# Kernel tuning notes

Hardware: AMD Instinct MI355X
Metric: run time of the kernel (lower is better)

## Reference

```python
import jax, jax.numpy as jnp
import numpy as np
from jax import lax

B, C, L, O, H, W = 256, 768, 64, 768, 9, 9
C2, C3 = 2 * C // 3, C // 3  # convh_2 / convl_1 output channels


def _c1x1(x, w, b):
    # 1x1 conv, w: (out,in), x: (b,in,h,w)
    return jnp.einsum('oc,bchw->bohw', w, x) + b[None, :, None, None]


def _conv3x3(x, w, b=None):
    out = lax.conv_general_dilated(x, w, (1, 1), 'SAME', dimension_numbers=('NCHW', 'OIHW', 'NCHW'))
    if b is not None:
        out = out + b[None, :, None, None]
    return out


def _cossim(a, b):
    # torch F.cosine_similarity over dim=1, eps=1e-8
    num = jnp.sum(a * b, axis=1)
    den = jnp.maximum(jnp.linalg.norm(a, axis=1) * jnp.linalg.norm(b, axis=1), 1e-8)
    return num / den


def _ufilt1d(x, size, axis):
    # scipy.ndimage.uniform_filter1d, mode='reflect' (== numpy 'symmetric')
    r = size // 2
    pad = [(r, r) if a == axis else (0, 0) for a in range(x.ndim)]
    xp = jnp.moveaxis(jnp.pad(x, pad, mode='symmetric'), axis, -1)
    c = jnp.cumsum(xp, axis=-1)
    c = jnp.concatenate([jnp.zeros_like(c[..., :1]), c], axis=-1)
    out = (c[..., size:] - c[..., :-size]) / size
    return jnp.moveaxis(out, -1, axis)


def _ufilt(x, size):
    # skimage ssim with channel_axis=1 on a (b,c,h,w) array treats (b,h,w) as
    # the 3 spatial dims (batch included!) and loops over channels.
    for ax in (0, 2, 3):
        x = _ufilt1d(x, size, ax)
    return x


def _ssim_map(x, y, win=7):
    NP = win ** 3  # 3 spatial dims (b,h,w)
    cov_norm = NP / (NP - 1.0)
    c1, c2 = 0.01 ** 2, 0.03 ** 2  # data_range = 1.0
    ux, uy = _ufilt(x, win), _ufilt(y, win)
    vx = cov_norm * (_ufilt(x * x, win) - ux * ux)
    vy = cov_norm * (_ufilt(y * y, win) - uy * uy)
    vxy = cov_norm * (_ufilt(x * y, win) - ux * uy)
    return ((2 * ux * uy + c1) * (2 * vxy + c2)) / ((ux * ux + uy * uy + c1) * (vx + vy + c2))


def setup_inputs() -> dict:
    key = jax.random.key(0)
    ks = jax.random.split(key, 40)
    n = lambda i, shape, s=1.0: jax.random.normal(ks[i], shape, jnp.float32) * s
    return {
        'x': n(0, (B, C, H, W)),
        'y': n(1, (B, L, H, W)),
        'w_convh1': n(2, (C, C), C ** -0.5), 'b_convh1': n(3, (C,), 0.01),
        'w_conv1_1': n(4, (C, C), C ** -0.5), 'b_conv1_1': n(5, (C,), 0.01),
        'w_convh2': n(6, (C2, C), C ** -0.5), 'b_convh2': n(7, (C2,), 0.01),
        'w_convl1': n(8, (C3, L), L ** -0.5), 'b_convl1': n(9, (C3,), 0.01),
        'w_convh3': n(10, (1, C), C ** -0.5), 'b_convh3': n(11, (1,), 0.01),
        'w_convl2': n(12, (1, L), L ** -0.5), 'b_convl2': n(13, (1,), 0.01),
        'w_conv1_2': n(14, (2, 2), 0.7), 'b_conv1_2': n(15, (2,), 0.01),
        'w_convl3': n(16, (2, L), L ** -0.5), 'b_convl3': n(17, (2,), 0.01),
        'w_cc1': n(18, (1, 2), 0.7), 'b_cc1': n(19, (1,), 0.01),
        'w_pool': n(20, (2, 1, 3, 3), 1.0 / 3.0), 'b_pool': n(21, (2,), 0.01),
        'w_fc1': n(22, (324, 324), 324 ** -0.5), 'b_fc1': n(23, (324,), 0.01),
        'w_fc2': n(24, (81, 324), 324 ** -0.5), 'b_fc2': n(25, (81,), 0.01),
        'w_bconv': n(26, (O, C, 3, 3), (C * 9) ** -0.5),
        'bn_gamma': 1.0 + n(27, (O,), 0.1), 'bn_beta': n(28, (O,), 0.1),
        'bn_mean': n(29, (O,), 0.1),
        'bn_var': 1.0 + 0.1 * jax.random.uniform(ks[30], (O,), jnp.float32),
    }


def reference(x, y, w_convh1, b_convh1, w_conv1_1, b_conv1_1, w_convh2, b_convh2,
              w_convl1, b_convl1, w_convh3, b_convh3, w_convl2, b_convl2,
              w_conv1_2, b_conv1_2, w_convl3, b_convl3, w_cc1, b_cc1,
              w_pool, b_pool, w_fc1, b_fc1, w_fc2, b_fc2,
              w_bconv, bn_gamma, bn_beta, bn_mean, bn_var):
    b = x.shape[0]
    fuse_1 = _c1x1(x, w_convh1, b_convh1)                                   # (b,C,9,9)
    fuse_2 = _c1x1(jnp.concatenate([_c1x1(x, w_convh2, b_convh2),
                                    _c1x1(y, w_convl1, b_convl1)], axis=1),
                   w_conv1_1, b_conv1_1)                                     # (b,C,9,9)
    fuse_3 = _c1x1(jnp.concatenate([_c1x1(x, w_convh3, b_convh3),
                                    _c1x1(y, w_convl2, b_convl2)], axis=1),
                   w_conv1_2, b_conv1_2)                                     # (b,2,9,9)
    fuse_4 = _c1x1(y, w_convl3, b_convl3)                                    # (b,2,9,9)
    cor_1 = _cossim(fuse_1, fuse_2)[:, None]                                 # (b,1,9,9)
    ssim_value = lax.stop_gradient(_ssim_map(fuse_3, fuse_4))                # detach() in torch
    fuse2_1 = fuse_1 + 0.5 * (1.0 - cor_1) * fuse_2
    fuse2_2 = _c1x1(fuse_4 + ssim_value * fuse_3, w_cc1, b_cc1)              # (b,1,9,9)
    cor2_1 = _cossim(fuse2_1, jnp.broadcast_to(fuse2_2, fuse2_1.shape))[:, None]
    fuse3_1 = fuse2_1 + 0.5 * (1.0 - cor2_1 + _c1x1(ssim_value, w_cc1, b_cc1)) * fuse2_2
    # fuse2_2 has 1 channel -> channel mean == channel max == fuse2_2
    xc = jnp.concatenate([fuse2_2, _conv3x3(fuse2_2, w_pool, b_pool), fuse2_2], axis=1)  # (b,4,9,9)
    xc = xc.reshape(b, -1)
    h1 = jax.nn.gelu(xc @ w_fc1.T + b_fc1, approximate=False)
    xweight = jax.nn.leaky_relu(h1 @ w_fc2.T + b_fc2, 0.01).reshape(b, 1, H, W)
    xout = xweight * fuse3_1 + fuse3_1
    xout = _conv3x3(xout, w_bconv)
    scale = (bn_gamma / jnp.sqrt(bn_var + 1e-5))[None, :, None, None]
    xout = (xout - bn_mean[None, :, None, None]) * scale + bn_beta[None, :, None, None]
    return jax.nn.leaky_relu(xout, 0.01)
```

## Files before the change

### kernel.cpp

```cpp
#include <hip/hip_runtime.h>
#include <hip/hip_bf16.h>
#include <math.h>

#define BATCH 256
#define CCH 768
#define LCH 64
#define PP 81

typedef __attribute__((ext_vector_type(8))) short short8v;
typedef __attribute__((ext_vector_type(4))) float f32x4;

__global__ __launch_bounds__(256) void kw_compose(
    const float* __restrict__ W11, const float* __restrict__ Wh2,
    const float* __restrict__ Wl1, const float* __restrict__ bh2,
    const float* __restrict__ bl1, const float* __restrict__ b11,
    const float* __restrict__ Wh1,
    __hip_bfloat16* __restrict__ WAp, __hip_bfloat16* __restrict__ WBp,
    __hip_bfloat16* __restrict__ Wh1p, float* __restrict__ beff)
{
    int o = blockIdx.x;
    int t = threadIdx.x;
    int ot = o >> 4, l15o = o & 15;
    const float* w11row = W11 + (size_t)o * CCH;
    for (int c = t; c < CCH; c += 256) {
        float s = 0.f;
        for (int k = 0; k < 512; ++k) s = fmaf(w11row[k], Wh2[(size_t)k*CCH + c], s);
        int ch = c >> 5, kg = (c >> 3) & 3, j = c & 7;
        size_t idx = (((size_t)ot*24 + ch) << 9) + (size_t)(kg*16 + l15o)*8 + j;
        WAp[idx]  = __float2bfloat16(s);
        Wh1p[idx] = __float2bfloat16(Wh1[(size_t)o*CCH + c]);
    }
    if (t < LCH) {
        float s = 0.f;
        for (int k = 0; k < 256; ++k) s = fmaf(w11row[512+k], Wl1[k*LCH + t], s);
        int ch = t >> 5, kg = (t >> 3) & 3, j = t & 7;
        size_t idx = (((size_t)ot*2 + ch) << 9) + (size_t)(kg*16 + l15o)*8 + j;
        WBp[idx] = __float2bfloat16(s);
    }
    if (t == 0) {
        float s = b11[o];
        for (int k = 0; k < 512; ++k) s = fmaf(w11row[k], bh2[k], s);
        for (int k = 0; k < 256; ++k) s = fmaf(w11row[512+k], bl1[k], s);
        beff[o] = s;
    }
}

__global__ __launch_bounds__(256) void k_wprep(
    const float* __restrict__ Wb, __hip_bfloat16* __restrict__ Wp)
{
    int ot = blockIdx.x;
    int i  = blockIdx.y*256 + threadIdx.x;
    int oi = i / 96, c8 = i - oi*96;
    const float* src = Wb + ((size_t)(ot*16 + oi)*CCH + c8*8)*9;
    int ch = c8 >> 2;
    int lane8 = (((c8 & 3)*16) + oi)*8;
    #pragma unroll
    for (int t = 0; t < 9; ++t) {
        short8v v;
        #pragma unroll
        for (int j = 0; j < 8; ++j) {
            __hip_bfloat16 h = __float2bfloat16(src[j*9 + t]);
            v[j] = __builtin_bit_cast(short, h);
        }
        *(short8v*)(Wp + ((((size_t)(t*48 + ot))*24 + ch) << 9) + lane8) = v;
    }
}

__global__ __launch_bounds__(256) void k_fcprep(
    const float* __restrict__ Wfc1, const float* __restrict__ Wfc2,
    float* __restrict__ T1, float* __restrict__ T2)
{
    int n = blockIdx.x*256 + threadIdx.x;
    if (n < 324*324) { int i = n / 324, j = n - i*324; T1[(size_t)j*324 + i] = Wfc1[n]; }
    if (n < 81*324)  { int q = n / 324, j = n - q*324; T2[(size_t)j*81 + q]  = Wfc2[n]; }
}

__global__ __launch_bounds__(256) void k_xprep_f34(
    const float* __restrict__ x, const float* __restrict__ y,
    const float* __restrict__ wh3, const float* __restrict__ bh3,
    const float* __restrict__ wl2, const float* __restrict__ bl2,
    const float* __restrict__ W12, const float* __restrict__ b12,
    const float* __restrict__ Wl3, const float* __restrict__ bl3,
    __hip_bfloat16* __restrict__ xT, __hip_bfloat16* __restrict__ yT,
    float* __restrict__ f3, float* __restrict__ f4, float* __restrict__ Af)
{
    int b = blockIdx.x;
    int tid = threadIdx.x;
    __shared__ float ls[64][82];
    __shared__ float red[243][4];
    __shared__ float zz[10][81];
    __shared__ float tb[10][81];
    int q = tid / 81, p81 = tid - q*81;
    bool act = tid < 243;
    float sx = 0.f;
    for (int c0 = 0; c0 < CCH; c0 += 64) {
        __syncthreads();
        for (int i = tid; i < 64*81; i += 256) {
            int c = i / 81, p = i - c*81;
            ls[c][p] = x[((size_t)b*CCH + c0 + c)*PP + p];
        }
        __syncthreads();
        for (int i = tid; i < 81*64; i += 256) {
            int p = i >> 6, c = i & 63;
            xT[((size_t)b*PP + p)*CCH + c0 + c] = __float2bfloat16(ls[c][p]);
        }
        if (act)
            for (int c = q; c < 64; c += 3)
                sx = fmaf(wh3[c0+c], ls[c][p81], sx);
    }
    __syncthreads();
    for (int i = tid; i < 64*81; i += 256) {
        int c = i / 81, p = i - c*81;
        ls[c][p] = y[((size_t)b*LCH + c)*PP + p];
    }
    __syncthreads();
    for (int i = tid; i < 81*64; i += 256) {
        int p = i >> 6, c = i & 63;
        yT[((size_t)b*PP + p)*LCH + c] = __float2bfloat16(ls[c][p]);
    }
    float sy = 0.f, s40 = 0.f, s41 = 0.f;
    if (act) {
        for (int c = q; c < 64; c += 3) {
            float v = ls[c][p81];
            sy  = fmaf(wl2[c], v, sy);
            s40 = fmaf(Wl3[c], v, s40);
            s41 = fmaf(Wl3[LCH+c], v, s41);
        }
        red[tid][0]=sx; red[tid][1]=sy; red[tid][2]=s40; red[tid][3]=s41;
    }
    __syncthreads();
    if (tid < 81) {
        float SX  = red[tid][0]+red[tid+81][0]+red[tid+162][0];
        float SY  = red[tid][1]+red[tid+81][1]+red[tid+162][1];
        float S40 = red[tid][2]+red[tid+81][2]+red[tid+162][2];
        float S41 = red[tid][3]+red[tid+81][3]+red[tid+162][3];
        float t3a = SX + bh3[0];
        float t3b = SY + bl2[0];
        float f30 = W12[0]*t3a + W12[1]*t3b + b12[0];
        float f31 = W12[2]*t3a + W12[3]*t3b + b12[1];
        float f40 = S40 + bl3[0];
        float f41 = S41 + bl3[1];
        f3[(b*2+0)*PP+tid] = f30; f3[(b*2+1)*PP+tid] = f31;
        f4[(b*2+0)*PP+tid] = f40; f4[(b*2+1)*PP+tid] = f41;
        zz[0][tid]=f30; zz[1][tid]=f40; zz[2][tid]=f30*f30; zz[3][tid]=f40*f40; zz[4][tid]=f30*f40;
        zz[5][tid]=f31; zz[6][tid]=f41; zz[7][tid]=f31*f31; zz[8][tid]=f41*f41; zz[9][tid]=f31*f41;
    }
    __syncthreads();
    for (int i = tid; i < 10*81; i += 256) {
        int f = i / 81, p = i - f*81;
        int yy = p/9, xx = p - yy*9;
        float s = 0.f;
        #pragma unroll
        for (int d = -3; d <= 3; ++d) {
            int j = xx + d;
            j = (j < 0) ? (-1-j) : ((j > 8) ? (17-j) : j);
            s += zz[f][yy*9+j];
        }
        tb[f][p] = s * (1.f/7.f);
    }
    __syncthreads();
    for (int i = tid; i < 10*81; i += 256) {
        int f = i / 81, p = i - f*81;
        int yy = p/9, xx = p - yy*9;
        float s = 0.f;
        #pragma unroll
        for (int d = -3; d <= 3; ++d) {
            int j = yy + d;
            j = (j < 0) ? (-1-j) : ((j > 8) ? (17-j) : j);
            s += tb[f][j*9+xx];
        }
        Af[((size_t)b*10 + f)*81 + p] = s * (1.f/7.f);
    }
}

__global__ __launch_bounds__(256) void k_ssim_b2(
    const float* __restrict__ A, float* __restrict__ U)
{
    int col0 = blockIdx.x * 32;
    int tid = threadIdx.x;
    __shared__ float lsb[256][33];
    for (int i = tid; i < 256*32; i += 256) {
        int j = i >> 5, cc = i & 31;
        int col = col0 + cc;
        lsb[j][cc] = (col < 810) ? A[(size_t)j*810 + col] : 0.f;
    }
    __syncthreads();
    for (int i = tid; i < 256*32; i += 256) {
        int b = i >> 5, cc = i & 31;
        float s = 0.f;
        #pragma unroll
        for (int d = -3; d <= 3; ++d) {
            int j = b + d;
            j = (j < 0) ? (-1-j) : ((j > 255) ? (511-j) : j);
            s += lsb[j][cc];
        }
        int col = col0 + cc;
        if (col < 810) U[(size_t)b*810 + col] = s * (1.f/7.f);
    }
}

__global__ __launch_bounds__(128) void k_fc(
    const float* __restrict__ U, const float* __restrict__ f3,
    const float* __restrict__ f4, const float* __restrict__ wcc,
    const float* __restrict__ bcc,
    const float* __restrict__ wpool, const float* __restrict__ bpool,
    const float* __restrict__ T1, const float* __restrict__ bfc1,
    const float* __restrict__ T2, const float* __restrict__ bfc2,
    float* __restrict__ f22, float* __restrict__ ccs,
    float* __restrict__ xw)
{
    int b = blockIdx.x;
    int tid = threadIdx.x;
    __shared__ float xc[324];
    __shared__ float h1[324];
    __shared__ float pr[2][81], ps[2][81];
    const float cov = 343.f/342.f, C1c = 1e-4f, C2c = 9e-4f;
    for (int i = tid; i < 162; i += 128) {
        int k = i / 81, p = i - k*81;
        const float* u = U + (size_t)b*810 + (k*5)*81 + p;
        float ux = u[0], uy = u[81], uxx = u[162], uyy = u[243], uxy = u[324];
        float vx = cov*(uxx - ux*ux), vy = cov*(uyy - uy*uy), vxy = cov*(uxy - ux*uy);
        float S = ((2.f*ux*uy + C1c)*(2.f*vxy + C2c)) /
                  ((ux*ux + uy*uy + C1c)*(vx + vy + C2c));
        float a = f4[(b*2+k)*81+p] + S*f3[(b*2+k)*81+p];
        pr[k][p] = wcc[k]*a;
        ps[k][p] = wcc[k]*S;
    }
    __syncthreads();
    if (tid < 81) {
        float fv = pr[0][tid] + pr[1][tid] + bcc[0];
        float cv = ps[0][tid] + ps[1][tid] + bcc[0];
        f22[b*81+tid] = fv;
        ccs[b*81+tid] = cv;
        xc[tid] = fv; xc[243+tid] = fv;
    }
    __syncthreads();
    for (int i = tid; i < 162; i += 128) {
        int k = i / 81, p = i - k*81;
        int yy = p/9, xx = p - yy*9;
        float s = bpool[k];
        #pragma unroll
        for (int dy = -1; dy <= 1; ++dy)
            #pragma unroll
            for (int dx = -1; dx <= 1; ++dx) {
                int Y = yy+dy, X = xx+dx;
                if (Y >= 0 && Y < 9 && X >= 0 && X < 9)
                    s = fmaf(wpool[k*9 + (dy+1)*3 + (dx+1)], xc[Y*9+X], s);
            }
        xc[81+i] = s;
    }
    __syncthreads();
    for (int i = tid; i < 324; i += 128) {
        float s = bfc1[i];
        for (int j = 0; j < 324; ++j) s = fmaf(T1[(size_t)j*324 + i], xc[j], s);
        h1[i] = 0.5f*s*(1.f + erff(s*0.70710678118654752f));
    }
    __syncthreads();
    for (int qq = tid; qq < 81; qq += 128) {
        float s = bfc2[qq];
        for (int j = 0; j < 324; ++j) s = fmaf(T2[(size_t)j*81 + qq], h1[j], s);
        xw[b*81+qq] = (s > 0.f) ? s : 0.01f*s;
    }
}

__global__ __launch_bounds__(256, 3) void k_fuse12_mfma(
    const __hip_bfloat16* __restrict__ xT,
    const __hip_bfloat16* __restrict__ yT,
    const __hip_bfloat16* __restrict__ Wh1p,
    const __hip_bfloat16* __restrict__ WAp,
    const __hip_bfloat16* __restrict__ WBp,
    const float* __restrict__ bh1, const float* __restrict__ beff,
    __hip_bfloat16* __restrict__ f1, __hip_bfloat16* __restrict__ f2)
{
    int oy = blockIdx.x;
    int b  = blockIdx.y;
    int tid = threadIdx.x;
    int w    = tid >> 6;
    int g    = w >> 1;
    int nh   = w & 1;
    int lane = tid & 63;
    int l15  = lane & 15;
    int kg   = lane >> 4;

    __shared__ __align__(16) __hip_bfloat16 ls[82*40];
    if (tid < 20) *(uint32_t*)&ls[81*40 + 2*tid] = 0u;

    int spoff[3];
    #pragma unroll
    for (int nl = 0; nl < 3; ++nl) {
        int p = (nh*3 + nl)*16 + l15;
        int sp = (p < PP) ? p : 81;
        spoff[nl] = sp*40 + kg*8;
    }

    f32x4 acc[6][3];
    #pragma unroll
    for (int m = 0; m < 6; ++m)
        #pragma unroll
        for (int nl = 0; nl < 3; ++nl)
            acc[m][nl] = (f32x4){0.f,0.f,0.f,0.f};

    const __hip_bfloat16* xb = xT + (size_t)b*PP*CCH;
    const __hip_bfloat16* Wsel = g ? WAp : Wh1p;
    int otb = oy*6;

    for (int ch = 0; ch < 24; ++ch) {
        int c0 = ch*32;
        __syncthreads();
        for (int i = tid; i < 81*4; i += 256) {
            int p = i >> 2, cp = i & 3;
            *(uint4*)&ls[p*40 + cp*8] = *(const uint4*)&xb[(size_t)p*CCH + c0 + cp*8];
        }
        __syncthreads();
        short8v a[6];
        #pragma unroll
        for (int m = 0; m < 6; ++m)
            a[m] = *(const short8v*)(Wsel + ((((size_t)(otb + m))*24 + ch) << 9) + (lane<<3));
        #pragma unroll
        for (int nl = 0; nl < 3; ++nl) {
            short8v bf = *(const short8v*)&ls[spoff[nl]];
            #pragma unroll
            for (int m = 0; m < 6; ++m)
                acc[m][nl] = __builtin_amdgcn_mfma_f32_16x16x32_bf16(a[m], bf, acc[m][nl], 0, 0, 0);
        }
    }

    const __hip_bfloat16* yb = yT + (size_t)b*PP*LCH;
    for (int ch2 = 0; ch2 < 2; ++ch2) {
        int l0 = ch2*32;
        __syncthreads();
        for (int i = tid; i < 81*4; i += 256) {
            int p = i >> 2, cp = i & 3;
            *(uint4*)&ls[p*40 + cp*8] = *(const uint4*)&yb[(size_t)p*LCH + l0 + cp*8];
        }
        __syncthreads();
        if (g == 1) {
            short8v a[6];
            #pragma unroll
            for (int m = 0; m < 6; ++m)
                a[m] = *(const short8v*)(WBp + ((((size_t)(otb + m))*2 + ch2) << 9) + (lane<<3));
            #pragma unroll
            for (int nl = 0; nl < 3; ++nl) {
                short8v bf = *(const short8v*)&ls[spoff[nl]];
                #pragma unroll
                for (int m = 0; m < 6; ++m)
                    acc[m][nl] = __builtin_amdgcn_mfma_f32_16x16x32_bf16(a[m], bf, acc[m][nl], 0, 0, 0);
            }
        }
    }

    __hip_bfloat16* dst = g ? f2 : f1;
    const float* bias = g ? beff : bh1;
    #pragma unroll
    for (int m = 0; m < 6; ++m) {
        #pragma unroll
        for (int r = 0; r < 4; ++r) {
            int o = (otb + m)*16 + kg*4 + r;
            float bb = bias[o];
            #pragma unroll
            for (int nl = 0; nl < 3; ++nl) {
                int p = (nh*3 + nl)*16 + l15;
                if (p < PP)
                    dst[((size_t)b*CCH + o)*PP + p] = __float2bfloat16(acc[m][nl][r] + bb);
            }
        }
    }
}

__global__ __launch_bounds__(256) void k_finalize(
    const __hip_bfloat16* __restrict__ f1, const __hip_bfloat16* __restrict__ f2,
    const float* __restrict__ f22, const float* __restrict__ ccs,
    const float* __restrict__ xw,
    __hip_bfloat16* __restrict__ inb)
{
    int b = blockIdx.x;
    int tid = threadIdx.x;
    __shared__ float red[243][5];
    __shared__ float sal[81], sga[81], scm[81];
    __shared__ float ls[64][82];
    bool act = tid < 243;
    float Sxx=0.f, Syy=0.f, Sxy=0.f, Sx=0.f, Sy=0.f;
    const __hip_bfloat16* A = f1 + (size_t)b*CCH*PP;
    const __hip_bfloat16* C = f2 + (size_t)b*CCH*PP;
    if (act) {
        for (int c0 = 0; c0 < CCH; c0 += 3) {
            float u = __bfloat162float(A[(size_t)c0*PP + tid]);
            float v = __bfloat162float(C[(size_t)c0*PP + tid]);
            Sxx = fmaf(u,u,Sxx); Syy = fmaf(v,v,Syy); Sxy = fmaf(u,v,Sxy);
            Sx += u; Sy += v;
        }
        red[tid][0]=Sxx; red[tid][1]=Syy; red[tid][2]=Sxy; red[tid][3]=Sx; red[tid][4]=Sy;
    }
    __syncthreads();
    if (tid < 81) {
        float xx = red[tid][0]+red[tid+81][0]+red[tid+162][0];
        float yy = red[tid][1]+red[tid+81][1]+red[tid+162][1];
        float xy = red[tid][2]+red[tid+81][2]+red[tid+162][2];
        float sx = red[tid][3]+red[tid+81][3]+red[tid+162][3];
        float sy = red[tid][4]+red[tid+81][4]+red[tid+162][4];
        float cor1 = xy / fmaxf(sqrtf(xx)*sqrtf(yy), 1e-8f);
        float al = 0.5f*(1.f - cor1);
        float sum21 = sx + al*sy;
        float n21 = sqrtf(fmaxf(xx + 2.f*al*xy + al*al*yy, 0.f));
        int t = b*81 + tid;
        float fv = f22[t];
        float cor2 = (fv * sum21) / fmaxf(n21 * 27.712812921102035f * fabsf(fv), 1e-8f);
        float be = 0.5f*(1.f - cor2 + ccs[t]);
        sal[tid] = al;
        sga[tid] = be * fv;
        scm[tid] = 1.f + xw[t];
    }
    for (int c0 = 0; c0 < CCH; c0 += 64) {
        __syncthreads();
        for (int i = tid; i < 64*81; i += 256) {
            int c = i / 81, p = i - c*81;
            size_t gidx = ((size_t)b*CCH + c0 + c)*PP + p;
            float u = __bfloat162float(f1[gidx]);
            float v = __bfloat162float(f2[gidx]);
            ls[c][p] = scm[p]*(u + sal[p]*v + sga[p]);
        }
        __syncthreads();
        for (int i = tid; i < 81*64; i += 256) {
            int p = i >> 6, c = i & 63;
            inb[((size_t)b*PP + p)*CCH + c0 + c] = __float2bfloat16(ls[c][p]);
        }
    }
}

__global__ __launch_bounds__(128, 3) void k_bconv_mfma(
    const __hip_bfloat16* __restrict__ inb,
    const __hip_bfloat16* __restrict__ Wp,
    const float* __restrict__ bn_g, const float* __restrict__ bn_b,
    const float* __restrict__ bn_m, const float* __restrict__ bn_v,
    float* __restrict__ out)
{
    int oy = blockIdx.x;
    int b  = blockIdx.y;
    int tid = threadIdx.x;
    int w    = tid >> 6;
    int lane = tid & 63;
    int l15  = lane & 15;
    int kg   = lane >> 4;

    __shared__ __align__(16) __hip_bfloat16 ls[82*40];
    if (tid < 20) *(uint32_t*)&ls[81*40 + 2*tid] = 0u;

    int spoff[9][3];
    #pragma unroll
    for (int t = 0; t < 9; ++t) {
        int dy = t/3 - 1, dx = t%3 - 1;
        #pragma unroll
        for (int nl = 0; nl < 3; ++nl) {
            int p = (w*3 + nl)*16 + l15;
            int yy = p/9, xx = p - yy*9;
            int Y = yy + dy, X = xx + dx;
            bool ok = (p < PP) && (Y >= 0) && (Y < 9) && (X >= 0) && (X < 9);
            int sp = ok ? (Y*9 + X) : 81;
            spoff[t][nl] = sp*40 + kg*8;
        }
    }

    f32x4 acc[6][3];
    #pragma unroll
    for (int m = 0; m < 6; ++m)
        #pragma unroll
        for (int nl = 0; nl < 3; ++nl)
            acc[m][nl] = (f32x4){0.f,0.f,0.f,0.f};

    const __hip_bfloat16* inbb = inb + (size_t)b*PP*CCH;
    int otb = oy*6;

    for (int ch = 0; ch < 24; ++ch) {
        int c0 = ch*32;
        __syncthreads();
        for (int i = tid; i < 81*4; i += 128) {
            int p = i >> 2, cp = i & 3;
            *(uint4*)&ls[p*40 + cp*8] = *(const uint4*)&inbb[(size_t)p*CCH + c0 + cp*8];
        }
        __syncthreads();
        #pragma unroll
        for (int t = 0; t < 9; ++t) {
            short8v a[6];
            #pragma unroll
            for (int m = 0; m < 6; ++m)
                a[m] = *(const short8v*)(Wp + (((size_t)(t*48 + otb + m)*24 + ch) << 9) + (lane<<3));
            #pragma unroll
            for (int nl = 0; nl < 3; ++nl) {
                short8v bf = *(const short8v*)&ls[spoff[t][nl]];
                #pragma unroll
                for (int m = 0; m < 6; ++m)
                    acc[m][nl] = __builtin_amdgcn_mfma_f32_16x16x32_bf16(a[m], bf, acc[m][nl], 0, 0, 0);
            }
        }
    }

    #pragma unroll
    for (int m = 0; m < 6; ++m) {
        #pragma unroll
        for (int r = 0; r < 4; ++r) {
            int o = (otb + m)*16 + kg*4 + r;
            float sc = bn_g[o] * rsqrtf(bn_v[o] + 1e-5f);
            float mn = bn_m[o], bt = bn_b[o];
            #pragma unroll
            for (int nl = 0; nl < 3; ++nl) {
                int p = (w*3 + nl)*16 + l15;
                if (p < PP) {
                    float v = (acc[m][nl][r] - mn) * sc + bt;
                    out[((size_t)b*CCH + o)*PP + p] = (v > 0.f) ? v : 0.01f*v;
                }
            }
        }
    }
}

extern "C" void kernel_launch(void* const* d_in, const int* in_sizes, int n_in,
                              void* d_out, int out_size, void* d_ws, size_t ws_size,
                              hipStream_t stream)
{
    (void)in_sizes; (void)n_in; (void)out_size; (void)ws_size;
    const float* x    = (const float*)d_in[0];
    const float* y    = (const float*)d_in[1];
    const float* Wh1  = (const float*)d_in[2];
    const float* bh1  = (const float*)d_in[3];
    const float* W11  = (const float*)d_in[4];
    const float* b11  = (const float*)d_in[5];
    const float* Wh2  = (const float*)d_in[6];
    const float* bh2  = (const float*)d_in[7];
    const float* Wl1  = (const float*)d_in[8];
    const float* bl1  = (const float*)d_in[9];
    const float* wh3  = (const float*)d_in[10];
    const float* bh3  = (const float*)d_in[11];
    const float* wl2  = (const float*)d_in[12];
    const float* bl2  = (const float*)d_in[13];
    const float* W12  = (const float*)d_in[14];
    const float* b12  = (const float*)d_in[15];
    const float* Wl3  = (const float*)d_in[16];
    const float* bl3  = (const float*)d_in[17];
    const float* wcc  = (const float*)d_in[18];
    const float* bcc  = (const float*)d_in[19];
    const float* wpool= (const float*)d_in[20];
    const float* bpool= (const float*)d_in[21];
    const float* Wfc1 = (const float*)d_in[22];
    const float* bfc1 = (const float*)d_in[23];
    const float* Wfc2 = (const float*)d_in[24];
    const float* bfc2 = (const float*)d_in[25];
    const float* Wb   = (const float*)d_in[26];
    const float* bng  = (const float*)d_in[27];
    const float* bnb  = (const float*)d_in[28];
    const float* bnm  = (const float*)d_in[29];
    const float* bnv  = (const float*)d_in[30];
    float* out = (float*)d_out;
    float* ws = (float*)d_ws;

    size_t off = 0;
    float* beff  = ws + off; off += CCH;
    float* f3    = ws + off; off += BATCH*2*PP;
    float* f4    = ws + off; off += BATCH*2*PP;
    float* Af    = ws + off; off += BATCH*10*PP;
    float* Uf    = ws + off; off += BATCH*10*PP;
    float* f22   = ws + off; off += BATCH*PP;
    float* ccs   = ws + off; off += BATCH*PP;
    float* xw    = ws + off; off += BATCH*PP;
    float* T1    = ws + off; off += 324*324;
    float* T2    = ws + off; off += 324*81;
    off = (off + 3) & ~(size_t)3;
    __hip_bfloat16* Wh1p = (__hip_bfloat16*)(ws + off); off += (size_t)48*24*512/2;
    __hip_bfloat16* WAp  = (__hip_bfloat16*)(ws + off); off += (size_t)48*24*512/2;
    __hip_bfloat16* WBp  = (__hip_bfloat16*)(ws + off); off += (size_t)48*2*512/2;
    __hip_bfloat16* yT   = (__hip_bfloat16*)(ws + off); off += (size_t)BATCH*PP*LCH/2;
    __hip_bfloat16* f1b  = (__hip_bfloat16*)(ws + off); off += (size_t)BATCH*CCH*PP/2;
    __hip_bfloat16* f2b  = (__hip_bfloat16*)(ws + off); off += (size_t)BATCH*CCH*PP/2;
    __hip_bfloat16* inb  = (__hip_bfloat16*)(ws + off); off += (size_t)BATCH*PP*CCH/2;
    __hip_bfloat16* Wp   = (__hip_bfloat16*)(ws + off); off += (size_t)9*48*24*512/2;
    __hip_bfloat16* xT = inb;

    kw_compose<<<dim3(CCH), dim3(256), 0, stream>>>(W11, Wh2, Wl1, bh2, bl1, b11, Wh1, WAp, WBp, Wh1p, beff);
    k_wprep<<<dim3(48, 6), dim3(256), 0, stream>>>(Wb, Wp);
    k_fcprep<<<dim3(411), dim3(256), 0, stream>>>(Wfc1, Wfc2, T1, T2);
    k_xprep_f34<<<dim3(BATCH), dim3(256), 0, stream>>>(x, y, wh3, bh3, wl2, bl2, W12, b12, Wl3, bl3, xT, yT, f3, f4, Af);
    k_ssim_b2<<<dim3(26), dim3(256), 0, stream>>>(Af, Uf);
    k_fc<<<dim3(BATCH), dim3(128), 0, stream>>>(Uf, f3, f4, wcc, bcc, wpool, bpool, T1, bfc1, T2, bfc2, f22, ccs, xw);
    k_fuse12_mfma<<<dim3(8, BATCH), dim3(256), 0, stream>>>(xT, yT, Wh1p, WAp, WBp, bh1, beff, f1b, f2b);
    k_finalize<<<dim3(BATCH), dim3(256), 0, stream>>>(f1b, f2b, f22, ccs, xw, inb);
    k_bconv_mfma<<<dim3(8, BATCH), dim3(128), 0, stream>>>(inb, Wp, bng, bnb, bnm, bnv, out);
}
```

Measured before the change: 811.0 us.

## Repack activations into swizzled channel-chunk tiles and double-buffer LDS via direct global-to-LDS loads

```diff
diff --git a/kernel.cpp b/kernel.cpp
--- a/kernel.cpp
+++ b/kernel.cpp
@@ -6,9 +6,14 @@
 #define CCH 768
 #define LCH 64
 #define PP 81
+#define CHW 3072
 
 typedef __attribute__((ext_vector_type(8))) short short8v;
 typedef __attribute__((ext_vector_type(4))) float f32x4;
+
+#define GLL16(gp, lp) __builtin_amdgcn_global_load_lds( \
+    (const __attribute__((address_space(1))) void*)(gp), \
+    (__attribute__((address_space(3))) void*)(lp), 16, 0, 0)
 
 __global__ __launch_bounds__(256) void kw_compose(
     const float* __restrict__ W11, const float* __restrict__ Wh2,
@@ -81,7 +86,7 @@
     const float* __restrict__ wl2, const float* __restrict__ bl2,
     const float* __restrict__ W12, const float* __restrict__ b12,
     const float* __restrict__ Wl3, const float* __restrict__ bl3,
-    __hip_bfloat16* __restrict__ xT, __hip_bfloat16* __restrict__ yT,
+    __hip_bfloat16* __restrict__ xT2, __hip_bfloat16* __restrict__ yT2,
     float* __restrict__ f3, float* __restrict__ f4, float* __restrict__ Af)
 {
     int b = blockIdx.x;
@@ -92,8 +97,17 @@
     __shared__ float tb[10][81];
     int q = tid / 81, p81 = tid - q*81;
     bool act = tid < 243;
+    for (int i = tid; i < 24*32; i += 256) {
+        int ch = i >> 5, c = i & 31;
+        xT2[(((size_t)b*24 + ch)*96 + 81)*32 + c] = __float2bfloat16(0.f);
+    }
+    if (tid < 2*32) {
+        int ch = tid >> 5, c = tid & 31;
+        yT2[(((size_t)b*2 + ch)*96 + 81)*32 + c] = __float2bfloat16(0.f);
+    }
     float sx = 0.f;
     for (int c0 = 0; c0 < CCH; c0 += 64) {
+        int ch0 = c0 >> 5;
         __syncthreads();
         for (int i = tid; i < 64*81; i += 256) {
             int c = i / 81, p = i - c*81;
@@ -102,7 +116,10 @@
         __syncthreads();
         for (int i = tid; i < 81*64; i += 256) {
             int p = i >> 6, c = i & 63;
-            xT[((size_t)b*PP + p)*CCH + c0 + c] = __float2bfloat16(ls[c][p]);
+            int ch = ch0 + (c >> 5), cc = c & 31;
+            int s = cc >> 3, j = cc & 7;
+            int slot = s ^ ((p >> 1) & 3);
+            xT2[(((size_t)b*24 + ch)*96 + p)*32 + slot*8 + j] = __float2bfloat16(ls[c][p]);
         }
         if (act)
             for (int c = q; c < 64; c += 3)
@@ -116,7 +133,10 @@
     __syncthreads();
     for (int i = tid; i < 81*64; i += 256) {
         int p = i >> 6, c = i & 63;
-        yT[((size_t)b*PP + p)*LCH + c] = __float2bfloat16(ls[c][p]);
+        int ch = c >> 5, cc = c & 31;
+        int s = cc >> 3, j = cc & 7;
+        int slot = s ^ ((p >> 1) & 3);
+        yT2[(((size_t)b*2 + ch)*96 + p)*32 + slot*8 + j] = __float2bfloat16(ls[c][p]);
     }
     float sy = 0.f, s40 = 0.f, s41 = 0.f;
     if (act) {
@@ -264,8 +284,8 @@
 }
 
 __global__ __launch_bounds__(256, 3) void k_fuse12_mfma(
-    const __hip_bfloat16* __restrict__ xT,
-    const __hip_bfloat16* __restrict__ yT,
+    const __hip_bfloat16* __restrict__ xT2,
+    const __hip_bfloat16* __restrict__ yT2,
     const __hip_bfloat16* __restrict__ Wh1p,
     const __hip_bfloat16* __restrict__ WAp,
     const __hip_bfloat16* __restrict__ WBp,
@@ -282,15 +302,14 @@
     int l15  = lane & 15;
     int kg   = lane >> 4;
 
-    __shared__ __align__(16) __hip_bfloat16 ls[82*40];
-    if (tid < 20) *(uint32_t*)&ls[81*40 + 2*tid] = 0u;
+    __shared__ __align__(16) __hip_bfloat16 ls[2*CHW];
 
     int spoff[3];
     #pragma unroll
     for (int nl = 0; nl < 3; ++nl) {
         int p = (nh*3 + nl)*16 + l15;
         int sp = (p < PP) ? p : 81;
-        spoff[nl] = sp*40 + kg*8;
+        spoff[nl] = sp*32 + ((kg ^ ((sp >> 1) & 3)) << 3);
     }
 
     f32x4 acc[6][3];
@@ -300,53 +319,58 @@
         for (int nl = 0; nl < 3; ++nl)
             acc[m][nl] = (f32x4){0.f,0.f,0.f,0.f};
 
-    const __hip_bfloat16* xb = xT + (size_t)b*PP*CCH;
+    const __hip_bfloat16* xb = xT2 + (size_t)b*24*CHW;
+    const __hip_bfloat16* yb = yT2 + (size_t)b*2*CHW;
     const __hip_bfloat16* Wsel = g ? WAp : Wh1p;
     int otb = oy*6;
 
-    for (int ch = 0; ch < 24; ++ch) {
-        int c0 = ch*32;
-        __syncthreads();
-        for (int i = tid; i < 81*4; i += 256) {
-            int p = i >> 2, cp = i & 3;
-            *(uint4*)&ls[p*40 + cp*8] = *(const uint4*)&xb[(size_t)p*CCH + c0 + cp*8];
-        }
-        __syncthreads();
-        short8v a[6];
-        #pragma unroll
-        for (int m = 0; m < 6; ++m)
-            a[m] = *(const short8v*)(Wsel + ((((size_t)(otb + m))*24 + ch) << 9) + (lane<<3));
-        #pragma unroll
-        for (int nl = 0; nl < 3; ++nl) {
-            short8v bf = *(const short8v*)&ls[spoff[nl]];
+    #pragma unroll
+    for (int k = 0; k < 2; ++k) {
+        int it = w + 4*k;
+        if (it < 6) GLL16(xb + it*512 + lane*8, &ls[it*512]);
+    }
+    __syncthreads();
+    int cur = 0;
+    for (int ch = 0; ch < 26; ++ch) {
+        if (ch < 25) {
+            const __hip_bfloat16* src = (ch+1 < 24) ? (xb + (size_t)(ch+1)*CHW)
+                                                    : (yb + (size_t)(ch+1-24)*CHW);
+            __hip_bfloat16* dst = &ls[(cur^1)*CHW];
+            #pragma unroll
+            for (int k = 0; k < 2; ++k) {
+                int it = w + 4*k;
+                if (it < 6) GLL16(src + it*512 + lane*8, dst + it*512);
+            }
+        }
+        const __hip_bfloat16* lb = &ls[cur*CHW];
+        if (ch < 24) {
+            short8v a[6];
             #pragma unroll
             for (int m = 0; m < 6; ++m)
-                acc[m][nl] = __builtin_amdgcn_mfma_f32_16x16x32_bf16(a[m], bf, acc[m][nl], 0, 0, 0);
-        }
-    }
-
-    const __hip_bfloat16* yb = yT + (size_t)b*PP*LCH;
-    for (int ch2 = 0; ch2 < 2; ++ch2) {
-        int l0 = ch2*32;
-        __syncthreads();
-        for (int i = tid; i < 81*4; i += 256) {
-            int p = i >> 2, cp = i & 3;
-            *(uint4*)&ls[p*40 + cp*8] = *(const uint4*)&yb[(size_t)p*LCH + l0 + cp*8];
-        }
-        __syncthreads();
-        if (g == 1) {
-            short8v a[6];
-            #pragma unroll
-            for (int m = 0; m < 6; ++m)
-                a[m] = *(const short8v*)(WBp + ((((size_t)(otb + m))*2 + ch2) << 9) + (lane<<3));
+                a[m] = *(const short8v*)(Wsel + ((((size_t)(otb + m))*24 + ch) << 9) + (lane<<3));
             #pragma unroll
             for (int nl = 0; nl < 3; ++nl) {
-                short8v bf = *(const short8v*)&ls[spoff[nl]];
+                short8v bf = *(const short8v*)&lb[spoff[nl]];
                 #pragma unroll
                 for (int m = 0; m < 6; ++m)
                     acc[m][nl] = __builtin_amdgcn_mfma_f32_16x16x32_bf16(a[m], bf, acc[m][nl], 0, 0, 0);
             }
-        }
+        } else if (g == 1) {
+            int ch2 = ch - 24;
+            short8v a[6];
+            #pragma unroll
+            for (int m = 0; m < 6; ++m)
+                a[m] = *(const short8v*)(WBp + ((((size_t)(otb + m))*2 + ch2) << 9) + (lane<<3));
+            #pragma unroll
+            for (int nl = 0; nl < 3; ++nl) {
+                short8v bf = *(const short8v*)&lb[spoff[nl]];
+                #pragma unroll
+                for (int m = 0; m < 6; ++m)
+                    acc[m][nl] = __builtin_amdgcn_mfma_f32_16x16x32_bf16(a[m], bf, acc[m][nl], 0, 0, 0);
+            }
+        }
+        __syncthreads();
+        cur ^= 1;
     }
 
     __hip_bfloat16* dst = g ? f2 : f1;
@@ -371,13 +395,17 @@
     const __hip_bfloat16* __restrict__ f1, const __hip_bfloat16* __restrict__ f2,
     const float* __restrict__ f22, const float* __restrict__ ccs,
     const float* __restrict__ xw,
-    __hip_bfloat16* __restrict__ inb)
+    __hip_bfloat16* __restrict__ inb2)
 {
     int b = blockIdx.x;
     int tid = threadIdx.x;
     __shared__ float red[243][5];
     __shared__ float sal[81], sga[81], scm[81];
     __shared__ float ls[64][82];
+    for (int i = tid; i < 24*32; i += 256) {
+        int ch = i >> 5, c = i & 31;
+        inb2[(((size_t)b*24 + ch)*96 + 81)*32 + c] = __float2bfloat16(0.f);
+    }
     bool act = tid < 243;
     float Sxx=0.f, Syy=0.f, Sxy=0.f, Sx=0.f, Sy=0.f;
     const __hip_bfloat16* A = f1 + (size_t)b*CCH*PP;
@@ -411,6 +439,7 @@
         scm[tid] = 1.f + xw[t];
     }
     for (int c0 = 0; c0 < CCH; c0 += 64) {
+        int ch0 = c0 >> 5;
         __syncthreads();
         for (int i = tid; i < 64*81; i += 256) {
             int c = i / 81, p = i - c*81;
@@ -422,13 +451,16 @@
         __syncthreads();
         for (int i = tid; i < 81*64; i += 256) {
             int p = i >> 6, c = i & 63;
-            inb[((size_t)b*PP + p)*CCH + c0 + c] = __float2bfloat16(ls[c][p]);
+            int ch = ch0 + (c >> 5), cc = c & 31;
+            int s = cc >> 3, j = cc & 7;
+            int slot = s ^ ((p >> 1) & 3);
+            inb2[(((size_t)b*24 + ch)*96 + p)*32 + slot*8 + j] = __float2bfloat16(ls[c][p]);
         }
     }
 }
 
 __global__ __launch_bounds__(128, 3) void k_bconv_mfma(
-    const __hip_bfloat16* __restrict__ inb,
+    const __hip_bfloat16* __restrict__ inb2,
     const __hip_bfloat16* __restrict__ Wp,
     const float* __restrict__ bn_g, const float* __restrict__ bn_b,
     const float* __restrict__ bn_m, const float* __restrict__ bn_v,
@@ -442,8 +474,7 @@
     int l15  = lane & 15;
     int kg   = lane >> 4;
 
-    __shared__ __align__(16) __hip_bfloat16 ls[82*40];
-    if (tid < 20) *(uint32_t*)&ls[81*40 + 2*tid] = 0u;
+    __shared__ __align__(16) __hip_bfloat16 ls[2*CHW];
 
     int spoff[9][3];
     #pragma unroll
@@ -456,7 +487,7 @@
             int Y = yy + dy, X = xx + dx;
             bool ok = (p < PP) && (Y >= 0) && (Y < 9) && (X >= 0) && (X < 9);
             int sp = ok ? (Y*9 + X) : 81;
-            spoff[t][nl] = sp*40 + kg*8;
+            spoff[t][nl] = sp*32 + ((kg ^ ((sp >> 1) & 3)) << 3);
         }
     }
 
@@ -467,17 +498,27 @@
         for (int nl = 0; nl < 3; ++nl)
             acc[m][nl] = (f32x4){0.f,0.f,0.f,0.f};
 
-    const __hip_bfloat16* inbb = inb + (size_t)b*PP*CCH;
+    const __hip_bfloat16* img = inb2 + (size_t)b*24*CHW;
     int otb = oy*6;
 
+    #pragma unroll
+    for (int k = 0; k < 3; ++k) {
+        int it = w + 2*k;
+        GLL16(img + it*512 + lane*8, &ls[it*512]);
+    }
+    __syncthreads();
+    int cur = 0;
     for (int ch = 0; ch < 24; ++ch) {
-        int c0 = ch*32;
-        __syncthreads();
-        for (int i = tid; i < 81*4; i += 128) {
-            int p = i >> 2, cp = i & 3;
-            *(uint4*)&ls[p*40 + cp*8] = *(const uint4*)&inbb[(size_t)p*CCH + c0 + cp*8];
-        }
-        __syncthreads();
+        if (ch < 23) {
+            const __hip_bfloat16* src = img + (size_t)(ch+1)*CHW;
+            __hip_bfloat16* dst = &ls[(cur^1)*CHW];
+            #pragma unroll
+            for (int k = 0; k < 3; ++k) {
+                int it = w + 2*k;
+                GLL16(src + it*512 + lane*8, dst + it*512);
+            }
+        }
+        const __hip_bfloat16* lb = &ls[cur*CHW];
         #pragma unroll
         for (int t = 0; t < 9; ++t) {
             short8v a[6];
@@ -486,12 +527,14 @@
                 a[m] = *(const short8v*)(Wp + (((size_t)(t*48 + otb + m)*24 + ch) << 9) + (lane<<3));
             #pragma unroll
             for (int nl = 0; nl < 3; ++nl) {
-                short8v bf = *(const short8v*)&ls[spoff[t][nl]];
+                short8v bf = *(const short8v*)&lb[spoff[t][nl]];
                 #pragma unroll
                 for (int m = 0; m < 6; ++m)
                     acc[m][nl] = __builtin_amdgcn_mfma_f32_16x16x32_bf16(a[m], bf, acc[m][nl], 0, 0, 0);
             }
         }
+        __syncthreads();
+        cur ^= 1;
     }
 
     #pragma unroll
@@ -565,22 +608,23 @@
     float* T2    = ws + off; off += 324*81;
     off = (off + 3) & ~(size_t)3;
     __hip_bfloat16* Wh1p = (__hip_bfloat16*)(ws + off); off += (size_t)48*24*512/2;
-    __hip_bfloat16* WAp  = (__hip_bfloat16*)(ws + off); off += (size_t)48*24*512/2;
+    __hip_bfloat16* WAp  = (__hip_bfloat16*)(ws + off); off += (size_t)48*2*512/2 + (size_t)48*22*512/2;
     __hip_bfloat16* WBp  = (__hip_bfloat16*)(ws + off); off += (size_t)48*2*512/2;
-    __hip_bfloat16* yT   = (__hip_bfloat16*)(ws + off); off += (size_t)BATCH*PP*LCH/2;
+    __hip_bfloat16* yT2  = (__hip_bfloat16*)(ws + off); off += (size_t)BATCH*2*CHW/2;
     __hip_bfloat16* f1b  = (__hip_bfloat16*)(ws + off); off += (size_t)BATCH*CCH*PP/2;
-    __hip_bfloat16* f2b  = (__hip_bfloat16*)(ws + off); off += (size_t)BATCH*CCH*PP/2;
-    __hip_bfloat16* inb  = (__hip_bfloat16*)(ws + off); off += (size_t)BATCH*PP*CCH/2;
+    __hip_bfloat16* f2b  = (__hip_bfloat16*)(ws + off); off += (size_t)BATCH*CCH*PP/2 + 1;
+    off = (off + 3) & ~(size_t)3;
+    __hip_bfloat16* inb2 = (__hip_bfloat16*)(ws + off); off += (size_t)BATCH*24*CHW/2;
     __hip_bfloat16* Wp   = (__hip_bfloat16*)(ws + off); off += (size_t)9*48*24*512/2;
-    __hip_bfloat16* xT = inb;
+    __hip_bfloat16* xT2 = inb2;
 
     kw_compose<<<dim3(CCH), dim3(256), 0, stream>>>(W11, Wh2, Wl1, bh2, bl1, b11, Wh1, WAp, WBp, Wh1p, beff);
     k_wprep<<<dim3(48, 6), dim3(256), 0, stream>>>(Wb, Wp);
     k_fcprep<<<dim3(411), dim3(256), 0, stream>>>(Wfc1, Wfc2, T1, T2);
-    k_xprep_f34<<<dim3(BATCH), dim3(256), 0, stream>>>(x, y, wh3, bh3, wl2, bl2, W12, b12, Wl3, bl3, xT, yT, f3, f4, Af);
+    k_xprep_f34<<<dim3(BATCH), dim3(256), 0, stream>>>(x, y, wh3, bh3, wl2, bl2, W12, b12, Wl3, bl3, xT2, yT2, f3, f4, Af);
     k_ssim_b2<<<dim3(26), dim3(256), 0, stream>>>(Af, Uf);
     k_fc<<<dim3(BATCH), dim3(128), 0, stream>>>(Uf, f3, f4, wcc, bcc, wpool, bpool, T1, bfc1, T2, bfc2, f22, ccs, xw);
-    k_fuse12_mfma<<<dim3(8, BATCH), dim3(256), 0, stream>>>(xT, yT, Wh1p, WAp, WBp, bh1, beff, f1b, f2b);
-    k_finalize<<<dim3(BATCH), dim3(256), 0, stream>>>(f1b, f2b, f22, ccs, xw, inb);
-    k_bconv_mfma<<<dim3(8, BATCH), dim3(128), 0, stream>>>(inb, Wp, bng, bnb, bnm, bnv, out);
-}
+    k_fuse12_mfma<<<dim3(8, BATCH), dim3(256), 0, stream>>>(xT2, yT2, Wh1p, WAp, WBp, bh1, beff, f1b, f2b);
+    k_finalize<<<dim3(BATCH), dim3(256), 0, stream>>>(f1b, f2b, f22, ccs, xw, inb2);
+    k_bconv_mfma<<<dim3(8, BATCH), dim3(128), 0, stream>>>(inb2, Wp, bng, bnb, bnm, bnv, out);
+}
```

Measured after the change: 922.8 us. 1.14x slower.
